# Kernel optimization log

Measured on AMD Instinct MI355X. Metric: run time of the kernel, lower is better.

The kernel has to match this reference:

```python
import jax, jax.numpy as jnp
import numpy as np

SHAPE = (192, 192, 192)


def _trilinear_sample(img, z, y, x):
    # img: [B,C,D,H,W]; z,y,x: [B,D,H,W] absolute voxel coords (align_corners=True,
    # zero padding outside the volume, matching F.grid_sample defaults in vroc).
    B, C, D, H, W = img.shape
    imgf = img.reshape(B, C, -1)
    z0 = jnp.floor(z); y0 = jnp.floor(y); x0 = jnp.floor(x)
    wz = z - z0; wy = y - y0; wx = x - x0
    z0i = z0.astype(jnp.int32); y0i = y0.astype(jnp.int32); x0i = x0.astype(jnp.int32)
    z1i = z0i + 1; y1i = y0i + 1; x1i = x0i + 1

    def gather(iz, iy, ix):
        valid = ((iz >= 0) & (iz < D) & (iy >= 0) & (iy < H) & (ix >= 0) & (ix < W))
        lin = ((jnp.clip(iz, 0, D - 1) * H + jnp.clip(iy, 0, H - 1)) * W
               + jnp.clip(ix, 0, W - 1)).reshape(B, 1, -1)
        v = jnp.take_along_axis(imgf, jnp.broadcast_to(lin, (B, C, D * H * W)), axis=2)
        return v.reshape(B, C, D, H, W) * valid.reshape(B, 1, D, H, W).astype(img.dtype)

    def w(a, b, c):
        return (a * b * c)[:, None]  # [B,1,D,H,W]

    out = (gather(z0i, y0i, x0i) * w(1 - wz, 1 - wy, 1 - wx)
           + gather(z0i, y0i, x1i) * w(1 - wz, 1 - wy, wx)
           + gather(z0i, y1i, x0i) * w(1 - wz, wy, 1 - wx)
           + gather(z0i, y1i, x1i) * w(1 - wz, wy, wx)
           + gather(z1i, y0i, x0i) * w(wz, 1 - wy, 1 - wx)
           + gather(z1i, y0i, x1i) * w(wz, 1 - wy, wx)
           + gather(z1i, y1i, x0i) * w(wz, wy, 1 - wx)
           + gather(z1i, y1i, x1i) * w(wz, wy, wx))
    return out


def _warp(moving_image, vector_field):
    # SpatialTransformer: identity grid + displacement (voxel units), trilinear sample.
    B, C, D, H, W = moving_image.shape
    dt = moving_image.dtype
    gz, gy, gx = jnp.meshgrid(jnp.arange(D, dtype=dt), jnp.arange(H, dtype=dt),
                              jnp.arange(W, dtype=dt), indexing='ij')
    z = gz[None] + vector_field[:, 0]
    y = gy[None] + vector_field[:, 1]
    x = gx[None] + vector_field[:, 2]
    return _trilinear_sample(moving_image, z, y, x)


def setup_inputs() -> dict:
    key = jax.random.key(0)
    k1, k2, k3, k4 = jax.random.split(key, 4)
    D, H, W = SHAPE
    moving_image = jax.random.normal(k1, (1, 1, D, H, W), dtype=jnp.float32)
    vector_field = jax.random.normal(k2, (1, 3, D, H, W), dtype=jnp.float32) * 3.0
    fixed_image = jax.random.normal(k3, (1, 1, D, H, W), dtype=jnp.float32)
    fixed_image_mask = jax.random.randint(k4, (1, 1, D, H, W), 0, 2).astype(bool)
    return {"moving_image": moving_image, "vector_field": vector_field,
            "fixed_image": fixed_image, "fixed_image_mask": fixed_image_mask}


def reference(moving_image, vector_field, fixed_image, fixed_image_mask):
    warped = _warp(moving_image, vector_field)
    m = fixed_image_mask.astype(warped.dtype)
    sq = (warped - fixed_image) ** 2
    # F.mse_loss(warped[mask], fixed[mask]) == mean of squared diff over masked voxels
    return jnp.sum(sq * m) / jnp.maximum(jnp.sum(m), 1.0)
```

## Files before the change

kernel.cpp:

```cpp
#include <hip/hip_runtime.h>
#include <hip/hip_fp16.h>

#define DD 192
#define HH 192
#define WW 192
#define NVOX (DD * HH * WW)

#define TX 32
#define TY 16
#define TZ 8
#define RSX 48
#define RSY 33
#define RSZ 25
#define ROWD 24
#define SLABD (RSY * ROWD)
#define RTOTH (RSX * RSY * RSZ)
#define RTOTD (RTOTH / 2)
#define NCHUNK (RTOTH / 8)
#define CHROW 6
#define CHSLAB (RSY * CHROW)
#define NT 1024
#define NROUND ((NCHUNK + NT - 1) / NT)
#define GRID 256

#define AS1 __attribute__((address_space(1)))
#define AS3 __attribute__((address_space(3)))

#define WAITCNT(n) asm volatile("s_waitcnt vmcnt(" #n ")" ::: "memory")

typedef float f32x4 __attribute__((ext_vector_type(4)));
typedef int   i32x4 __attribute__((ext_vector_type(4)));

__global__ __launch_bounds__(256) void conv_fp16(
    const float4* __restrict__ in, int4* __restrict__ out)
{
    const int i = blockIdx.x * 256 + threadIdx.x;
    const float4 a = in[2 * i];
    const float4 b = in[2 * i + 1];
    __half2 h0 = __floats2half2_rn(a.x, a.y);
    __half2 h1 = __floats2half2_rn(a.z, a.w);
    __half2 h2 = __floats2half2_rn(b.x, b.y);
    __half2 h3 = __floats2half2_rn(b.z, b.w);
    int4 o;
    o.x = *(int*)&h0; o.y = *(int*)&h1; o.z = *(int*)&h2; o.w = *(int*)&h3;
    out[i] = o;
}

struct Streams { f32x4 dz, dy, dx, f; i32x4 m; };

__device__ __forceinline__ void tile_coords_oct(
    int n, int OX, int OY, int OZ, int& tx, int& ty, int& tz)
{
    const int ox = n / 72;
    const int r  = n - ox * 72;
    const int oy = r / 12;
    tx = OX + ox;
    ty = OY + oy;
    tz = OZ + (r - oy * 12);
}

__device__ __forceinline__ void stage_tile(
    const ushort* __restrict__ movh, const ushort* __restrict__ zbuf,
    uint* sbufd, int x_lo, int y_lo, int z_lo, int tid)
{
    ushort* sbuf = (ushort*)sbufd;
    #pragma unroll
    for (int i = 0; i < NROUND; ++i) {
        const int q = tid + i * NT;
        if (q < NCHUNK) {
            const int rz = q / CHSLAB;
            const int rem = q - rz * CHSLAB;
            const int ry = rem / CHROW;
            const int k  = rem - ry * CHROW;
            const int gz = z_lo + rz, gy = y_lo + ry, gx = x_lo + 8 * k;
            const bool valid = ((unsigned)gz < DD) & ((unsigned)gy < HH) &
                               ((unsigned)gx < WW);
            const ushort* src = valid ? (movh + ((gz * HH + gy) * WW + gx)) : zbuf;
            const int qb = i * NT + (tid & ~63);
            __builtin_amdgcn_global_load_lds((AS1 void*)src,
                                             (AS3 void*)(sbuf + 8 * qb), 16, 0, 0);
        }
    }
}

__device__ __forceinline__ Streams prefetch_streams(
    const float* __restrict__ vf, const float* __restrict__ fix,
    const int* __restrict__ mask, int base)
{
    Streams s;
    s.dz = __builtin_nontemporal_load((const f32x4*)(vf + base));
    s.dy = __builtin_nontemporal_load((const f32x4*)(vf + NVOX + base));
    s.dx = __builtin_nontemporal_load((const f32x4*)(vf + 2 * NVOX + base));
    s.f  = __builtin_nontemporal_load((const f32x4*)(fix + base));
    s.m  = __builtin_nontemporal_load((const i32x4*)(mask + base));
    return s;
}

__device__ __forceinline__ void sample_accum(
    const uint* sdw, const ushort* __restrict__ movh,
    int gz, int gy, int gx, float dz, float dy, float dx,
    float f, int m, int x_lo, int y_lo, int z_lo,
    float& sq, float& cnt)
{
    const float z = (float)gz + dz, y = (float)gy + dy, x = (float)gx + dx;
    const float z0f = floorf(z), y0f = floorf(y), x0f = floorf(x);
    const float wz = z - z0f, wy = y - y0f, wx = x - x0f;
    const int z0 = (int)z0f, y0 = (int)y0f, x0 = (int)x0f;
    const int z0l = z0 - z_lo, y0l = y0 - y_lo, x0l = x0 - x_lo;
    const bool inbox = ((unsigned)z0l < RSZ - 1) & ((unsigned)y0l < RSY - 1) &
                       ((unsigned)x0l < RSX - 1);

    float v000, v001, v010, v011, v100, v101, v110, v111;
    if (inbox) {
        const int o = z0l * SLABD + y0l * ROWD + (x0l >> 1);
        const bool odd = (x0l & 1) != 0;
        const uint a00 = sdw[o];
        const uint b00 = sdw[o + 1];
        const uint a01 = sdw[o + ROWD];
        const uint b01 = sdw[o + ROWD + 1];
        const uint a10 = sdw[o + SLABD];
        const uint b10 = sdw[o + SLABD + 1];
        const uint a11 = sdw[o + SLABD + ROWD];
        const uint b11 = sdw[o + SLABD + ROWD + 1];
        auto pr = [&](uint A, uint B, float& l, float& r) {
            const float2 fa = __half22float2(*(const __half2*)&A);
            const float fb = __low2float(*(const __half2*)&B);
            l = odd ? fa.y : fa.x;
            r = odd ? fb   : fa.y;
        };
        pr(a00, b00, v000, v001);
        pr(a01, b01, v010, v011);
        pr(a10, b10, v100, v101);
        pr(a11, b11, v110, v111);
    } else {
        const int z1 = z0 + 1, y1 = y0 + 1, x1 = x0 + 1;
        const bool zi0 = (unsigned)z0 < DD, zi1 = (unsigned)z1 < DD;
        const bool yi0 = (unsigned)y0 < HH, yi1 = (unsigned)y1 < HH;
        const bool xi0 = (unsigned)x0 < WW, xi1 = (unsigned)x1 < WW;
        const int zc0 = min(max(z0, 0), DD - 1), zc1 = min(max(z1, 0), DD - 1);
        const int yc0 = min(max(y0, 0), HH - 1), yc1 = min(max(y1, 0), HH - 1);
        const int xc0 = min(max(x0, 0), WW - 1), xc1 = min(max(x1, 0), WW - 1);
        const int r00 = (zc0 * HH + yc0) * WW;
        const int r01 = (zc0 * HH + yc1) * WW;
        const int r10 = (zc1 * HH + yc0) * WW;
        const int r11 = (zc1 * HH + yc1) * WW;
        v000 = (zi0 & yi0 & xi0) ? __half2float(((const __half*)movh)[r00 + xc0]) : 0.0f;
        v001 = (zi0 & yi0 & xi1) ? __half2float(((const __half*)movh)[r00 + xc1]) : 0.0f;
        v010 = (zi0 & yi1 & xi0) ? __half2float(((const __half*)movh)[r01 + xc0]) : 0.0f;
        v011 = (zi0 & yi1 & xi1) ? __half2float(((const __half*)movh)[r01 + xc1]) : 0.0f;
        v100 = (zi1 & yi0 & xi0) ? __half2float(((const __half*)movh)[r10 + xc0]) : 0.0f;
        v101 = (zi1 & yi0 & xi1) ? __half2float(((const __half*)movh)[r10 + xc1]) : 0.0f;
        v110 = (zi1 & yi1 & xi0) ? __half2float(((const __half*)movh)[r11 + xc0]) : 0.0f;
        v111 = (zi1 & yi1 & xi1) ? __half2float(((const __half*)movh)[r11 + xc1]) : 0.0f;
    }

    const float c00 = v000 + (v001 - v000) * wx;
    const float c01 = v010 + (v011 - v010) * wx;
    const float c10 = v100 + (v101 - v100) * wx;
    const float c11 = v110 + (v111 - v110) * wx;
    const float c0 = c00 + (c01 - c00) * wy;
    const float c1 = c10 + (c11 - c10) * wy;
    const float warped = c0 + (c1 - c0) * wz;

    const float mm = (m != 0) ? 1.0f : 0.0f;
    const float diff = warped - f;
    sq += diff * diff * mm;
    cnt += mm;
}

__global__ __launch_bounds__(NT) void warp_mse_persist(
    const ushort* __restrict__ movh,
    const float* __restrict__ mov,
    const float* __restrict__ vf,
    const float* __restrict__ fix,
    const int* __restrict__ mask,
    const ushort* __restrict__ zbuf,
    float* __restrict__ acc,
    float* __restrict__ out)
{
    __shared__ uint sbufd[2][RTOTD + 8];
    __shared__ float s_sq[16], s_cnt[16];

    const int tid = threadIdx.x;
    const int b = blockIdx.x;
    const int xcd = b & 7;
    const int w   = b >> 3;
    const int start = w * 6 + min(w, 24);
    const int cnt_t = 6 + (w < 24 ? 1 : 0);
    const int OX = (xcd & 1) * 3;
    const int OY = ((xcd >> 1) & 1) * 6;
    const int OZ = ((xcd >> 2) & 1) * 12;

    const int lxg = (tid & 7) * 4;
    const int ly  = (tid >> 3) & 15;
    const int lz  = tid >> 7;

    float sq = 0.0f, cntm = 0.0f;

    int tx, ty, tz;
    tile_coords_oct(start, OX, OY, OZ, tx, ty, tz);
    stage_tile(movh, zbuf, sbufd[0], tx * TX - 8, ty * TY - 8, tz * TZ - 8, tid);
    Streams Scur = prefetch_streams(vf, fix, mask,
        ((tz * TZ + lz) * HH + ty * TY + ly) * WW + tx * TX + lxg);
    Streams Snxt = Scur;
    if (cnt_t > 1) {
        int nx, ny, nz;
        tile_coords_oct(start + 1, OX, OY, OZ, nx, ny, nz);
        stage_tile(movh, zbuf, sbufd[1], nx * TX - 8, ny * TY - 8, nz * TZ - 8, tid);
        Snxt = prefetch_streams(vf, fix, mask,
            ((nz * TZ + lz) * HH + ny * TY + ly) * WW + nx * TX + lxg);
        WAITCNT(14);
    } else {
        WAITCNT(5);
    }
    __builtin_amdgcn_s_barrier();
    __builtin_amdgcn_sched_barrier(0);

    for (int k = 0; k < cnt_t; ++k) {
        const int cur = k & 1;
        int cx, cy, cz;
        tile_coords_oct(start + k, OX, OY, OZ, cx, cy, cz);
        const int x_lo = cx * TX - 8, y_lo = cy * TY - 8, z_lo = cz * TZ - 8;
        const int gz = cz * TZ + lz, gy = cy * TY + ly, gx0 = cx * TX + lxg;
        const uint* sdw = sbufd[cur];

        sample_accum(sdw, movh, gz, gy, gx0,     Scur.dz.x, Scur.dy.x, Scur.dx.x,
                     Scur.f.x, Scur.m.x, x_lo, y_lo, z_lo, sq, cntm);
        sample_accum(sdw, movh, gz, gy, gx0 + 1, Scur.dz.y, Scur.dy.y, Scur.dx.y,
                     Scur.f.y, Scur.m.y, x_lo, y_lo, z_lo, sq, cntm);
        sample_accum(sdw, movh, gz, gy, gx0 + 2, Scur.dz.z, Scur.dy.z, Scur.dx.z,
                     Scur.f.z, Scur.m.z, x_lo, y_lo, z_lo, sq, cntm);
        sample_accum(sdw, movh, gz, gy, gx0 + 3, Scur.dz.w, Scur.dy.w, Scur.dx.w,
                     Scur.f.w, Scur.m.w, x_lo, y_lo, z_lo, sq, cntm);

        if (k + 1 < cnt_t) {
            __builtin_amdgcn_sched_barrier(0);
            __builtin_amdgcn_s_barrier();
            Streams Snew = Snxt;
            if (k + 2 < cnt_t) {
                int nx, ny, nz;
                tile_coords_oct(start + k + 2, OX, OY, OZ, nx, ny, nz);
                stage_tile(movh, zbuf, sbufd[cur],
                           nx * TX - 8, ny * TY - 8, nz * TZ - 8, tid);
                Snew = prefetch_streams(vf, fix, mask,
                    ((nz * TZ + lz) * HH + ny * TY + ly) * WW + nx * TX + lxg);
                WAITCNT(14);
            } else {
                WAITCNT(5);
            }
            __builtin_amdgcn_s_barrier();
            __builtin_amdgcn_sched_barrier(0);
            Scur = Snxt;
            Snxt = Snew;
        }
    }

    #pragma unroll
    for (int off = 32; off > 0; off >>= 1) {
        sq   += __shfl_down(sq, off, 64);
        cntm += __shfl_down(cntm, off, 64);
    }
    const int lane = tid & 63;
    const int wid = tid >> 6;
    if (lane == 0) { s_sq[wid] = sq; s_cnt[wid] = cntm; }
    __syncthreads();
    if (tid == 0) {
        float bsq = 0.0f, bcnt = 0.0f;
        #pragma unroll
        for (int i = 0; i < 16; ++i) { bsq += s_sq[i]; bcnt += s_cnt[i]; }
        atomicAdd(&acc[0], bsq);
        atomicAdd(&acc[1], bcnt);
        __threadfence();
        const unsigned old = atomicAdd((unsigned*)&acc[2], 1u);
        if (old == GRID - 1) {
            __threadfence();
            const float s = atomicAdd(&acc[0], 0.0f);
            const float c = atomicAdd(&acc[1], 0.0f);
            out[0] = s / fmaxf(c, 1.0f);
        }
    }
}

__global__ __launch_bounds__(256) void warp_mse_simple(
    const float* __restrict__ mov, const float* __restrict__ vf,
    const float* __restrict__ fix, const int* __restrict__ mask,
    float* __restrict__ acc)
{
    const int idx = blockIdx.x * 256 + threadIdx.x;
    float sq = 0.0f, cnt = 0.0f;
    if (idx < NVOX) {
        const int w = idx % WW;
        const int t = idx / WW;
        const int h = t % HH;
        const int d = t / HH;
        const float z = (float)d + vf[idx];
        const float y = (float)h + vf[NVOX + idx];
        const float x = (float)w + vf[2 * NVOX + idx];
        const float z0f = floorf(z), y0f = floorf(y), x0f = floorf(x);
        const float wz = z - z0f, wy = y - y0f, wx = x - x0f;
        const int z0 = (int)z0f, y0 = (int)y0f, x0 = (int)x0f;
        const int z1 = z0 + 1, y1 = y0 + 1, x1 = x0 + 1;
        const bool zi0 = (unsigned)z0 < DD, zi1 = (unsigned)z1 < DD;
        const bool yi0 = (unsigned)y0 < HH, yi1 = (unsigned)y1 < HH;
        const bool xi0 = (unsigned)x0 < WW, xi1 = (unsigned)x1 < WW;
        auto ld = [&](int iz, int iy, int ix, bool ok) -> float {
            return ok ? mov[(iz * HH + iy) * WW + ix] : 0.0f;
        };
        const float v000 = ld(z0, y0, x0, zi0 & yi0 & xi0);
        const float v001 = ld(z0, y0, x1, zi0 & yi0 & xi1);
        const float v010 = ld(z0, y1, x0, zi0 & yi1 & xi0);
        const float v011 = ld(z0, y1, x1, zi0 & yi1 & xi1);
        const float v100 = ld(z1, y0, x0, zi1 & yi0 & xi0);
        const float v101 = ld(z1, y0, x1, zi1 & yi0 & xi1);
        const float v110 = ld(z1, y1, x0, zi1 & yi1 & xi0);
        const float v111 = ld(z1, y1, x1, zi1 & yi1 & xi1);
        const float c00 = v000 + (v001 - v000) * wx;
        const float c01 = v010 + (v011 - v010) * wx;
        const float c10 = v100 + (v101 - v100) * wx;
        const float c11 = v110 + (v111 - v110) * wx;
        const float c0 = c00 + (c01 - c00) * wy;
        const float c1 = c10 + (c11 - c10) * wy;
        const float warped = c0 + (c1 - c0) * wz;
        const float m = (mask[idx] != 0) ? 1.0f : 0.0f;
        const float diff = warped - fix[idx];
        sq = diff * diff * m;
        cnt = m;
    }
    #pragma unroll
    for (int off = 32; off > 0; off >>= 1) {
        sq  += __shfl_down(sq, off, 64);
        cnt += __shfl_down(cnt, off, 64);
    }
    __shared__ float s_sq[4], s_cnt[4];
    const int lane = threadIdx.x & 63, wid = threadIdx.x >> 6;
    if (lane == 0) { s_sq[wid] = sq; s_cnt[wid] = cnt; }
    __syncthreads();
    if (threadIdx.x == 0) {
        atomicAdd(&acc[0], s_sq[0] + s_sq[1] + s_sq[2] + s_sq[3]);
        atomicAdd(&acc[1], s_cnt[0] + s_cnt[1] + s_cnt[2] + s_cnt[3]);
    }
}

__global__ void warp_mse_finalize(const float* __restrict__ acc, float* __restrict__ out) {
    out[0] = acc[0] / fmaxf(acc[1], 1.0f);
}

extern "C" void kernel_launch(void* const* d_in, const int* in_sizes, int n_in,
                              void* d_out, int out_size, void* d_ws, size_t ws_size,
                              hipStream_t stream) {
    const float* mov  = (const float*)d_in[0];
    const float* vf   = (const float*)d_in[1];
    const float* fix  = (const float*)d_in[2];
    const int*   mask = (const int*)d_in[3];
    float* acc = (float*)d_ws;
    float* out = (float*)d_out;

    hipMemsetAsync(d_ws, 0, 256, stream);

    const size_t need = 256 + (size_t)NVOX * 2;
    if (ws_size >= need) {
        ushort* movh = (ushort*)((char*)d_ws + 256);
        const ushort* zbuf = (const ushort*)((char*)d_ws + 64);
        conv_fp16<<<NVOX / (256 * 8), 256, 0, stream>>>(
            (const float4*)mov, (int4*)movh);
        warp_mse_persist<<<GRID, NT, 0, stream>>>(movh, mov, vf, fix, mask,
                                                  zbuf, acc, out);
    } else {
        warp_mse_simple<<<(NVOX + 255) / 256, 256, 0, stream>>>(mov, vf, fix, mask, acc);
        warp_mse_finalize<<<1, 1, 0, stream>>>(acc, out);
    }
}
```

Before: 217.2 us.

## Stage halo as a z-ring buffer of slabs reused across consecutive z tiles

Replaces the double-buffered full halo tile with a 32-slab circular LDS buffer indexed by global z. Tiles are walked as z-columns, so moving to the next z tile loads only 8 new slabs instead of the whole 25-slab halo, cutting global and LDS staging traffic. The trade-off is that the slab loads are no longer double-buffered ahead of compute: they are issued right after the barrier and waited on with vmcnt(5) or vmcnt(0) before the next tile starts. It also adds an odd algebraic no-op in the c11 interpolation.

New measurement: 246.9 us. +13.7%, slower.

```diff
diff --git a/kernel.cpp b/kernel.cpp
--- a/kernel.cpp
+++ b/kernel.cpp
@@ -12,15 +12,12 @@
 #define RSX 48
 #define RSY 33
 #define RSZ 25
+#define DEPTH 32
 #define ROWD 24
 #define SLABD (RSY * ROWD)
-#define RTOTH (RSX * RSY * RSZ)
-#define RTOTD (RTOTH / 2)
-#define NCHUNK (RTOTH / 8)
 #define CHROW 6
 #define CHSLAB (RSY * CHROW)
 #define NT 1024
-#define NROUND ((NCHUNK + NT - 1) / NT)
 #define GRID 256
 
 #define AS1 __attribute__((address_space(1)))
@@ -48,37 +45,45 @@
 
 struct Streams { f32x4 dz, dy, dx, f; i32x4 m; };
 
-__device__ __forceinline__ void tile_coords_oct(
-    int n, int OX, int OY, int OZ, int& tx, int& ty, int& tz)
-{
-    const int ox = n / 72;
-    const int r  = n - ox * 72;
-    const int oy = r / 12;
+__device__ __forceinline__ void tile_coords_col(
+    int n, int OX, int OY, int OZ, int& tx, int& ty, int& tz, int& tzi)
+{
+    const int c = n / 12;
+    tzi = n - c * 12;
+    const int ox = c / 6;
     tx = OX + ox;
-    ty = OY + oy;
-    tz = OZ + (r - oy * 12);
-}
-
-__device__ __forceinline__ void stage_tile(
+    ty = OY + (c - ox * 6);
+    tz = OZ + tzi;
+}
+
+__device__ __forceinline__ void stage_slabs(
     const ushort* __restrict__ movh, const ushort* __restrict__ zbuf,
-    uint* sbufd, int x_lo, int y_lo, int z_lo, int tid)
+    uint* sbufd, int x_lo, int y_lo, int z_first, int nslab, int tid)
 {
     ushort* sbuf = (ushort*)sbufd;
-    #pragma unroll
-    for (int i = 0; i < NROUND; ++i) {
-        const int q = tid + i * NT;
-        if (q < NCHUNK) {
-            const int rz = q / CHSLAB;
-            const int rem = q - rz * CHSLAB;
-            const int ry = rem / CHROW;
-            const int k  = rem - ry * CHROW;
-            const int gz = z_lo + rz, gy = y_lo + ry, gx = x_lo + 8 * k;
-            const bool valid = ((unsigned)gz < DD) & ((unsigned)gy < HH) &
-                               ((unsigned)gx < WW);
-            const ushort* src = valid ? (movh + ((gz * HH + gy) * WW + gx)) : zbuf;
-            const int qb = i * NT + (tid & ~63);
-            __builtin_amdgcn_global_load_lds((AS1 void*)src,
-                                             (AS3 void*)(sbuf + 8 * qb), 16, 0, 0);
+    const int sg = tid >> 7;
+    const int lq = tid & 127;
+    for (int it = 0; it < (nslab + 7) / 8; ++it) {
+        const int j = it * 8 + sg;
+        if (j < nslab) {
+            const int zg = z_first + j;
+            const int s  = zg & (DEPTH - 1);
+            #pragma unroll
+            for (int r = 0; r < 2; ++r) {
+                const int q = lq + r * 128;
+                if (q < CHSLAB) {
+                    const int ry = q / CHROW;
+                    const int k  = q - ry * CHROW;
+                    const int gy = y_lo + ry, gx = x_lo + 8 * k;
+                    const bool valid = ((unsigned)zg < DD) & ((unsigned)gy < HH) &
+                                       ((unsigned)gx < WW);
+                    const ushort* src = valid ? (movh + ((zg * HH + gy) * WW + gx))
+                                              : zbuf;
+                    const int cb = q & ~63;
+                    __builtin_amdgcn_global_load_lds((AS1 void*)src,
+                        (AS3 void*)(sbuf + s * (SLABD * 2) + cb * 8), 16, 0, 0);
+                }
+            }
         }
     }
 }
@@ -112,16 +117,18 @@
 
     float v000, v001, v010, v011, v100, v101, v110, v111;
     if (inbox) {
-        const int o = z0l * SLABD + y0l * ROWD + (x0l >> 1);
+        const int sb0 = (z0 & (DEPTH - 1)) * SLABD;
+        const int sb1 = ((z0 + 1) & (DEPTH - 1)) * SLABD;
+        const int ob = y0l * ROWD + (x0l >> 1);
         const bool odd = (x0l & 1) != 0;
-        const uint a00 = sdw[o];
-        const uint b00 = sdw[o + 1];
-        const uint a01 = sdw[o + ROWD];
-        const uint b01 = sdw[o + ROWD + 1];
-        const uint a10 = sdw[o + SLABD];
-        const uint b10 = sdw[o + SLABD + 1];
-        const uint a11 = sdw[o + SLABD + ROWD];
-        const uint b11 = sdw[o + SLABD + ROWD + 1];
+        const uint a00 = sdw[sb0 + ob];
+        const uint b00 = sdw[sb0 + ob + 1];
+        const uint a01 = sdw[sb0 + ob + ROWD];
+        const uint b01 = sdw[sb0 + ob + ROWD + 1];
+        const uint a10 = sdw[sb1 + ob];
+        const uint b10 = sdw[sb1 + ob + 1];
+        const uint a11 = sdw[sb1 + ob + ROWD];
+        const uint b11 = sdw[sb1 + ob + ROWD + 1];
         auto pr = [&](uint A, uint B, float& l, float& r) {
             const float2 fa = __half22float2(*(const __half2*)&A);
             const float fb = __low2float(*(const __half2*)&B);
@@ -157,7 +164,7 @@
     const float c00 = v000 + (v001 - v000) * wx;
     const float c01 = v010 + (v011 - v010) * wx;
     const float c10 = v100 + (v101 - v100) * wx;
-    const float c11 = v110 + (v111 - v110) * wx;
+    const float c11 = v110 + (v110 - v110) * wx + (v111 - v110) * wx;
     const float c0 = c00 + (c01 - c00) * wy;
     const float c1 = c10 + (c11 - c10) * wy;
     const float warped = c0 + (c1 - c0) * wz;
@@ -178,7 +185,7 @@
     float* __restrict__ acc,
     float* __restrict__ out)
 {
-    __shared__ uint sbufd[2][RTOTD + 8];
+    __shared__ uint sbufd[DEPTH * SLABD + 8];
     __shared__ float s_sq[16], s_cnt[16];
 
     const int tid = threadIdx.x;
@@ -197,32 +204,25 @@
 
     float sq = 0.0f, cntm = 0.0f;
 
-    int tx, ty, tz;
-    tile_coords_oct(start, OX, OY, OZ, tx, ty, tz);
-    stage_tile(movh, zbuf, sbufd[0], tx * TX - 8, ty * TY - 8, tz * TZ - 8, tid);
+    int tx, ty, tz, tzi;
+    tile_coords_col(start, OX, OY, OZ, tx, ty, tz, tzi);
+    stage_slabs(movh, zbuf, sbufd, tx * TX - 8, ty * TY - 8, tz * TZ - 8, RSZ, tid);
     Streams Scur = prefetch_streams(vf, fix, mask,
         ((tz * TZ + lz) * HH + ty * TY + ly) * WW + tx * TX + lxg);
-    Streams Snxt = Scur;
-    if (cnt_t > 1) {
-        int nx, ny, nz;
-        tile_coords_oct(start + 1, OX, OY, OZ, nx, ny, nz);
-        stage_tile(movh, zbuf, sbufd[1], nx * TX - 8, ny * TY - 8, nz * TZ - 8, tid);
-        Snxt = prefetch_streams(vf, fix, mask,
-            ((nz * TZ + lz) * HH + ny * TY + ly) * WW + nx * TX + lxg);
-        WAITCNT(14);
-    } else {
-        WAITCNT(5);
-    }
+    int nx, ny, nz, nzi;
+    tile_coords_col(start + 1, OX, OY, OZ, nx, ny, nz, nzi);
+    Streams Snxt = prefetch_streams(vf, fix, mask,
+        ((nz * TZ + lz) * HH + ny * TY + ly) * WW + nx * TX + lxg);
+    WAITCNT(10);
     __builtin_amdgcn_s_barrier();
     __builtin_amdgcn_sched_barrier(0);
 
     for (int k = 0; k < cnt_t; ++k) {
-        const int cur = k & 1;
-        int cx, cy, cz;
-        tile_coords_oct(start + k, OX, OY, OZ, cx, cy, cz);
+        int cx, cy, cz, czi;
+        tile_coords_col(start + k, OX, OY, OZ, cx, cy, cz, czi);
         const int x_lo = cx * TX - 8, y_lo = cy * TY - 8, z_lo = cz * TZ - 8;
         const int gz = cz * TZ + lz, gy = cy * TY + ly, gx0 = cx * TX + lxg;
-        const uint* sdw = sbufd[cur];
+        const uint* sdw = sbufd;
 
         sample_accum(sdw, movh, gz, gy, gx0,     Scur.dz.x, Scur.dy.x, Scur.dx.x,
                      Scur.f.x, Scur.m.x, x_lo, y_lo, z_lo, sq, cntm);
@@ -236,17 +236,25 @@
         if (k + 1 < cnt_t) {
             __builtin_amdgcn_sched_barrier(0);
             __builtin_amdgcn_s_barrier();
+            int px, py, pz, pzi;
+            tile_coords_col(start + k + 1, OX, OY, OZ, px, py, pz, pzi);
+            const int zlo1 = pz * TZ - 8;
+            if (czi != 11) {
+                stage_slabs(movh, zbuf, sbufd, px * TX - 8, py * TY - 8,
+                            zlo1 + 17, 8, tid);
+            } else {
+                stage_slabs(movh, zbuf, sbufd, px * TX - 8, py * TY - 8,
+                            zlo1, RSZ, tid);
+            }
             Streams Snew = Snxt;
             if (k + 2 < cnt_t) {
-                int nx, ny, nz;
-                tile_coords_oct(start + k + 2, OX, OY, OZ, nx, ny, nz);
-                stage_tile(movh, zbuf, sbufd[cur],
-                           nx * TX - 8, ny * TY - 8, nz * TZ - 8, tid);
+                int qx, qy, qz, qzi;
+                tile_coords_col(start + k + 2, OX, OY, OZ, qx, qy, qz, qzi);
                 Snew = prefetch_streams(vf, fix, mask,
-                    ((nz * TZ + lz) * HH + ny * TY + ly) * WW + nx * TX + lxg);
-                WAITCNT(14);
+                    ((qz * TZ + lz) * HH + qy * TY + ly) * WW + qx * TX + lxg);
+                WAITCNT(5);
             } else {
-                WAITCNT(5);
+                WAITCNT(0);
             }
             __builtin_amdgcn_s_barrier();
             __builtin_amdgcn_sched_barrier(0);
```
